# Optimization experiments

Hardware: AMD Instinct MI355X
Metric: run time of the kernel (lower is better)

Reference implementation:

```python
import jax, jax.numpy as jnp
import numpy as np

H, L, NB = 128, 2048, 64  # features, seq len, half state size (conj-symmetric N=128)


def _forward(u, x_re, x_im, Lambda_re, Lambda_im, B_re, B_im, C_re, C_im, D, d):
    Lam = (Lambda_re + 1j * Lambda_im).astype(jnp.complex64)   # (H, NB) discrete diag A
    B = (B_re + 1j * B_im).astype(jnp.complex64)               # (H, NB)
    C = (C_re + 1j * C_im).astype(jnp.complex64)               # (H, NB)
    x0 = (x_re + 1j * x_im).astype(jnp.complex64)              # (H, NB) initial state
    Hn, Ln = u.shape
    # scan elements (A_t, b_t, d_t); identity element (1, x0, False) prepended at t=0
    A = jnp.concatenate([jnp.ones((Hn, 1, NB), jnp.complex64),
                         jnp.broadcast_to(Lam[:, None, :], (Hn, Ln, NB))], axis=1)
    b = jnp.concatenate([x0[:, None, :],
                         B[:, None, :] * u[:, :, None].astype(jnp.complex64)], axis=1)
    dd = jnp.concatenate([jnp.zeros((1,), bool), d.astype(bool)])[None, :, None]  # (1, L+1, 1)

    def combine(lhs, rhs):
        # reset-aware associative combine: if right done-flag set, drop left contribution
        A_i, b_i, c_i = lhs
        A_j, b_j, c_j = rhs
        return (jnp.where(c_j, A_j, A_j * A_i),
                jnp.where(c_j, b_j, A_j * b_i + b_j),
                jnp.logical_or(c_i, c_j))

    _, xs, _ = jax.lax.associative_scan(combine, (A, b, dd), axis=1)
    xs = xs[:, 1:]                                             # (H, L, NB) hidden states
    # conj symmetry: y_t = 2*Re(C @ x_t) + D * u_t
    y = 2.0 * jnp.real(jnp.einsum('hn,hln->hl', C, xs)) + D[:, None] * u
    return y, xs[:, -1]


def setup_inputs():
    key = jax.random.key(0)
    ks = jax.random.split(key, 8)
    # stable ZOH-discretized HiPPO-like diagonal system (mirrors LSSL-f init)
    dts = jnp.logspace(-3.0, -1.0, H)                          # (H,) per-feature timescales
    k = jnp.arange(NB, dtype=jnp.float32)
    lam_c = -0.5 + 1j * jnp.pi * (2.0 * k + 1.0)               # (NB,) continuous poles
    lam_d = jnp.exp(dts[:, None] * lam_c[None, :]).astype(jnp.complex64)  # (H, NB), |.|<1
    Bc = ((jax.random.normal(ks[0], (NB,)) + 1j * jax.random.normal(ks[1], (NB,)))
          / jnp.sqrt(2.0 * NB)).astype(jnp.complex64)
    Bd = (((lam_d - 1.0) / lam_c[None, :]) * Bc[None, :]).astype(jnp.complex64)  # (H, NB)
    C = ((jax.random.normal(ks[2], (H, NB)) + 1j * jax.random.normal(ks[3], (H, NB)))
         / jnp.sqrt(float(NB))).astype(jnp.complex64)
    return {
        "u": jax.random.normal(ks[4], (H, L), jnp.float32),
        "x_re": jnp.zeros((H, NB), jnp.float32),
        "x_im": jnp.zeros((H, NB), jnp.float32),
        "Lambda_re": jnp.real(lam_d).astype(jnp.float32),
        "Lambda_im": jnp.imag(lam_d).astype(jnp.float32),
        "B_re": jnp.real(Bd).astype(jnp.float32),
        "B_im": jnp.imag(Bd).astype(jnp.float32),
        "C_re": jnp.real(C).astype(jnp.float32),
        "C_im": jnp.imag(C).astype(jnp.float32),
        "D": jax.random.normal(ks[5], (H,), jnp.float32),
        "d": jax.random.bernoulli(ks[6], 0.01, (L,)),
    }


def reference(u, x_re, x_im, Lambda_re, Lambda_im, B_re, B_im, C_re, C_im, D, d):
    return _forward(u, x_re, x_im, Lambda_re, Lambda_im, B_re, B_im, C_re, C_im, D, d)
```

## Files before the change

kernel.cpp:

```cpp
#include <hip/hip_runtime.h>

#define Hn 128
#define Ln 2048
#define NBn 64
#define K 64
#define G 32
#define PITCH 65


__global__ __launch_bounds__(64) void k1_summary(
    const float* __restrict__ u,
    const float* __restrict__ Lre,  const float* __restrict__ Lim,
    const float* __restrict__ Bre,  const float* __restrict__ Bim,
    const float* __restrict__ Cre,  const float* __restrict__ Cim,
    const int* __restrict__ dflag,
    float4* __restrict__ Sum)
{
    __shared__ float u_s[K];

    const int g = blockIdx.x, h = blockIdx.y, n = threadIdx.x;
    const int hn = h * NBn + n;
    const int l0 = g * K;

    const float lre = Lre[hn], lim = Lim[hn];
    const float br  = Bre[hn], bi  = Bim[hn];
    const float cr  = Cre[hn], ci  = Cim[hn];
    const float cbr2 = 2.f * (cr * br - ci * bi);
    const float cbi2 = 2.f * (cr * bi + ci * br);

    u_s[n] = u[h * Ln + l0 + n];
    const unsigned long long m = __ballot(dflag[l0 + n] != 0);
    __syncthreads();

    float wr = 0.f, wi = 0.f;
    if (m == 0ull) {
        #pragma unroll
        for (int k = 0; k < K; ++k) {
            const float uk = u_s[k];
            const float nr = fmaf(lre, wr, fmaf(-lim, wi, cbr2 * uk));
            const float ni = fmaf(lre, wi, fmaf( lim, wr, cbi2 * uk));
            wr = nr; wi = ni;
        }
    } else {
        #pragma unroll
        for (int k = 0; k < K; ++k) {
            const bool  rs  = (m >> k) & 1ull;
            const float lrk = rs ? 0.f : lre;
            const float lik = rs ? 0.f : lim;
            const float uk  = u_s[k];
            const float nr = fmaf(lrk, wr, fmaf(-lik, wi, cbr2 * uk));
            const float ni = fmaf(lrk, wi, fmaf( lik, wr, cbi2 * uk));
            wr = nr; wi = ni;
        }
    }

    float pr = lre, pi = lim;
    #pragma unroll
    for (int it = 0; it < 6; ++it) {
        const float sr2 = pr * pr - pi * pi;
        const float si2 = 2.f * pr * pi;
        pr = sr2; pi = si2;
    }
    if (m) { pr = 0.f; pi = 0.f; }
    Sum[(h * G + g) * NBn + n] = make_float4(pr, pi, wr, wi);
}

__global__ __launch_bounds__(64) void k2_combine(
    const float* __restrict__ x_re, const float* __restrict__ x_im,
    const float* __restrict__ Cre,  const float* __restrict__ Cim,
    const float4* __restrict__ Sum,
    float2* __restrict__ Sin,
    float* __restrict__ out)
{
    const int h = blockIdx.x, n = threadIdx.x;
    const int hn = h * NBn + n;
    const float cr = Cre[hn], ci = Cim[hn];
    const float x0r = x_re[hn], x0i = x_im[hn];
    float sre = 2.f * (cr * x0r - ci * x0i);
    float sim = 2.f * (cr * x0i + ci * x0r);
    #pragma unroll
    for (int g = 0; g < G; ++g) {
        const int idx = (h * G + g) * NBn + n;
        const float4 s = Sum[idx];
        Sin[idx] = make_float2(sre, sim);
        const float nr = fmaf(s.x, sre, fmaf(-s.y, sim, s.z));
        const float ni = fmaf(s.x, sim, fmaf( s.y, sre, s.w));
        sre = nr; sim = ni;
    }
    const float c2r = 2.f * cr, c2i = 2.f * ci;
    const float inv = 1.f / (c2r * c2r + c2i * c2i);
    float* xlast = out + Hn * Ln;
    xlast[2 * hn + 0] = (sre * c2r + sim * c2i) * inv;
    xlast[2 * hn + 1] = (sim * c2r - sre * c2i) * inv;
}

__global__ __launch_bounds__(64) void k3_rescan(
    const float* __restrict__ u,
    const float* __restrict__ Lre,  const float* __restrict__ Lim,
    const float* __restrict__ Bre,  const float* __restrict__ Bim,
    const float* __restrict__ Cre,  const float* __restrict__ Cim,
    const float* __restrict__ Dv,   const int* __restrict__ dflag,
    const float2* __restrict__ Sin,
    float* __restrict__ out)
{
    __shared__ float g_s[K * PITCH];
    __shared__ float u_s[K];

    const int g = blockIdx.x, h = blockIdx.y, n = threadIdx.x;
    const int hn = h * NBn + n;
    const int l0 = g * K;

    const float lre = Lre[hn], lim = Lim[hn];
    const float br  = Bre[hn], bi  = Bim[hn];
    const float cr  = Cre[hn], ci  = Cim[hn];
    const float Dh  = Dv[h];
    const float cbr2 = 2.f * (cr * br - ci * bi);
    const float cbi2 = 2.f * (cr * bi + ci * br);

    const float2 win = Sin[(h * G + g) * NBn + n];
    const float ul = u[h * Ln + l0 + n];
    u_s[n] = ul;
    const unsigned long long m = __ballot(dflag[l0 + n] != 0);
    __syncthreads();

    float wr = win.x, wi = win.y;
    if (m == 0ull) {
        #pragma unroll
        for (int k = 0; k < K; ++k) {
            const float uk = u_s[k];
            const float nr = fmaf(lre, wr, fmaf(-lim, wi, cbr2 * uk));
            const float ni = fmaf(lre, wi, fmaf( lim, wr, cbi2 * uk));
            wr = nr; wi = ni;
            g_s[k * PITCH + n] = wr;
        }
    } else {
        #pragma unroll
        for (int k = 0; k < K; ++k) {
            const bool  rs  = (m >> k) & 1ull;
            const float lrk = rs ? 0.f : lre;
            const float lik = rs ? 0.f : lim;
            const float uk  = u_s[k];
            const float nr = fmaf(lrk, wr, fmaf(-lik, wi, cbr2 * uk));
            const float ni = fmaf(lrk, wi, fmaf( lik, wr, cbi2 * uk));
            wr = nr; wi = ni;
            g_s[k * PITCH + n] = wr;
        }
    }
    __syncthreads();

    const float* row = g_s + n * PITCH;
    float a0 = 0.f, a1 = 0.f, a2 = 0.f, a3 = 0.f;
    #pragma unroll
    for (int k = 0; k < NBn; k += 4) {
        a0 += row[k + 0]; a1 += row[k + 1];
        a2 += row[k + 2]; a3 += row[k + 3];
    }
    out[h * Ln + l0 + n] = (a0 + a1) + (a2 + a3) + Dh * ul;
}

extern "C" void kernel_launch(void* const* d_in, const int* in_sizes, int n_in,
                              void* d_out, int out_size, void* d_ws, size_t ws_size,
                              hipStream_t stream) {
    const float* u    = (const float*)d_in[0];
    const float* x_re = (const float*)d_in[1];
    const float* x_im = (const float*)d_in[2];
    const float* Lre  = (const float*)d_in[3];
    const float* Lim  = (const float*)d_in[4];
    const float* Bre  = (const float*)d_in[5];
    const float* Bim  = (const float*)d_in[6];
    const float* Cre  = (const float*)d_in[7];
    const float* Cim  = (const float*)d_in[8];
    const float* Dv   = (const float*)d_in[9];
    const int*   dfl  = (const int*)d_in[10];
    float* out = (float*)d_out;

    const int HGN = Hn * G * NBn;
    float4* Sum = (float4*)d_ws;
    float2* Sin = (float2*)(Sum + HGN);

    dim3 grid(G, Hn);
    k1_summary<<<grid, 64, 0, stream>>>(u, Lre, Lim, Bre, Bim, Cre, Cim,
                                        dfl, Sum);
    k2_combine<<<Hn, 64, 0, stream>>>(x_re, x_im, Cre, Cim, Sum, Sin, out);
    k3_rescan<<<grid, 64, 0, stream>>>(u, Lre, Lim, Bre, Bim, Cre, Cim,
                                       Dv, dfl, Sin, out);
}
```

Measured before the change: 89.07 us.

## Fuse chunk summary and cross-chunk combine into one per-feature block

Merges the chunk-summary kernel and the sequential combine kernel into a single 1024-thread block per feature. Each of 16 waves computes two chunk summaries into shared memory, and wave 0 then runs the 32-step carry propagation from LDS. This removes one kernel launch and the global round-trip of the float4 summary buffer. In exchange, the first stage now runs only 128 blocks instead of 4096, and the serial combine runs on a single wave while the other 15 waves sit idle.

```diff
diff --git a/kernel.cpp b/kernel.cpp
--- a/kernel.cpp
+++ b/kernel.cpp
@@ -8,19 +8,22 @@
 #define PITCH 65
 
 
-__global__ __launch_bounds__(64) void k1_summary(
+__global__ __launch_bounds__(1024) void kA_sum_combine(
     const float* __restrict__ u,
+    const float* __restrict__ x_re, const float* __restrict__ x_im,
     const float* __restrict__ Lre,  const float* __restrict__ Lim,
     const float* __restrict__ Bre,  const float* __restrict__ Bim,
     const float* __restrict__ Cre,  const float* __restrict__ Cim,
     const int* __restrict__ dflag,
-    float4* __restrict__ Sum)
+    float2* __restrict__ Sin,
+    float* __restrict__ out)
 {
-    __shared__ float u_s[K];
+    __shared__ float  u_s[Ln];
+    __shared__ float4 b_s[G][NBn];
 
-    const int g = blockIdx.x, h = blockIdx.y, n = threadIdx.x;
+    const int h = blockIdx.x, tid = threadIdx.x;
+    const int w = tid >> 6, n = tid & 63;
     const int hn = h * NBn + n;
-    const int l0 = g * K;
 
     const float lre = Lre[hn], lim = Lim[hn];
     const float br  = Bre[hn], bi  = Bim[hn];
@@ -28,73 +31,78 @@
     const float cbr2 = 2.f * (cr * br - ci * bi);
     const float cbi2 = 2.f * (cr * bi + ci * br);
 
-    u_s[n] = u[h * Ln + l0 + n];
-    const unsigned long long m = __ballot(dflag[l0 + n] != 0);
+    u_s[tid]        = u[h * Ln + tid];
+    u_s[tid + 1024] = u[h * Ln + tid + 1024];
+
+    unsigned long long mk[2];
+    #pragma unroll
+    for (int jj = 0; jj < 2; ++jj)
+        mk[jj] = __ballot(dflag[(2 * w + jj) * K + n] != 0);
+
+    float l64r = lre, l64i = lim;
+    #pragma unroll
+    for (int it = 0; it < 6; ++it) {
+        const float a  = l64r * l64r - l64i * l64i;
+        const float b2 = 2.f * l64r * l64i;
+        l64r = a; l64i = b2;
+    }
+
     __syncthreads();
 
-    float wr = 0.f, wi = 0.f;
-    if (m == 0ull) {
+    #pragma unroll
+    for (int jj = 0; jj < 2; ++jj) {
+        const int j  = 2 * w + jj;
+        const int l0 = j * K;
+        const unsigned long long m = mk[jj];
+        float wr = 0.f, wi = 0.f;
+        if (m == 0ull) {
+            #pragma unroll
+            for (int k = 0; k < K; ++k) {
+                const float uk = u_s[l0 + k];
+                const float nr = fmaf(lre, wr, fmaf(-lim, wi, cbr2 * uk));
+                const float ni = fmaf(lre, wi, fmaf( lim, wr, cbi2 * uk));
+                wr = nr; wi = ni;
+            }
+        } else {
+            #pragma unroll
+            for (int k = 0; k < K; ++k) {
+                const bool  rs  = (m >> k) & 1ull;
+                const float lrk = rs ? 0.f : lre;
+                const float lik = rs ? 0.f : lim;
+                const float uk  = u_s[l0 + k];
+                const float nr = fmaf(lrk, wr, fmaf(-lik, wi, cbr2 * uk));
+                const float ni = fmaf(lrk, wi, fmaf( lik, wr, cbi2 * uk));
+                wr = nr; wi = ni;
+            }
+        }
+        const float ar = m ? 0.f : l64r;
+        const float ai = m ? 0.f : l64i;
+        b_s[j][n] = make_float4(ar, ai, wr, wi);
+    }
+    __syncthreads();
+
+    if (w == 0) {
+        const float x0r = x_re[hn], x0i = x_im[hn];
+        float sre = 2.f * (cr * x0r - ci * x0i);
+        float sim = 2.f * (cr * x0i + ci * x0r);
+        float2* sbase = Sin + h * G * NBn + n;
         #pragma unroll
-        for (int k = 0; k < K; ++k) {
-            const float uk = u_s[k];
-            const float nr = fmaf(lre, wr, fmaf(-lim, wi, cbr2 * uk));
-            const float ni = fmaf(lre, wi, fmaf( lim, wr, cbi2 * uk));
-            wr = nr; wi = ni;
+        for (int g = 0; g < G; ++g) {
+            const float4 s = b_s[g][n];
+            sbase[g * NBn] = make_float2(sre, sim);
+            const float nr = fmaf(s.x, sre, fmaf(-s.y, sim, s.z));
+            const float ni = fmaf(s.x, sim, fmaf( s.y, sre, s.w));
+            sre = nr; sim = ni;
         }
-    } else {
-        #pragma unroll
-        for (int k = 0; k < K; ++k) {
-            const bool  rs  = (m >> k) & 1ull;
-            const float lrk = rs ? 0.f : lre;
-            const float lik = rs ? 0.f : lim;
-            const float uk  = u_s[k];
-            const float nr = fmaf(lrk, wr, fmaf(-lik, wi, cbr2 * uk));
-            const float ni = fmaf(lrk, wi, fmaf( lik, wr, cbi2 * uk));
-            wr = nr; wi = ni;
-        }
+        const float c2r = 2.f * cr, c2i = 2.f * ci;
+        const float inv = 1.f / (c2r * c2r + c2i * c2i);
+        float* xlast = out + Hn * Ln;
+        xlast[2 * hn + 0] = (sre * c2r + sim * c2i) * inv;
+        xlast[2 * hn + 1] = (sim * c2r - sre * c2i) * inv;
     }
-
-    float pr = lre, pi = lim;
-    #pragma unroll
-    for (int it = 0; it < 6; ++it) {
-        const float sr2 = pr * pr - pi * pi;
-        const float si2 = 2.f * pr * pi;
-        pr = sr2; pi = si2;
-    }
-    if (m) { pr = 0.f; pi = 0.f; }
-    Sum[(h * G + g) * NBn + n] = make_float4(pr, pi, wr, wi);
 }
 
-__global__ __launch_bounds__(64) void k2_combine(
-    const float* __restrict__ x_re, const float* __restrict__ x_im,
-    const float* __restrict__ Cre,  const float* __restrict__ Cim,
-    const float4* __restrict__ Sum,
-    float2* __restrict__ Sin,
-    float* __restrict__ out)
-{
-    const int h = blockIdx.x, n = threadIdx.x;
-    const int hn = h * NBn + n;
-    const float cr = Cre[hn], ci = Cim[hn];
-    const float x0r = x_re[hn], x0i = x_im[hn];
-    float sre = 2.f * (cr * x0r - ci * x0i);
-    float sim = 2.f * (cr * x0i + ci * x0r);
-    #pragma unroll
-    for (int g = 0; g < G; ++g) {
-        const int idx = (h * G + g) * NBn + n;
-        const float4 s = Sum[idx];
-        Sin[idx] = make_float2(sre, sim);
-        const float nr = fmaf(s.x, sre, fmaf(-s.y, sim, s.z));
-        const float ni = fmaf(s.x, sim, fmaf( s.y, sre, s.w));
-        sre = nr; sim = ni;
-    }
-    const float c2r = 2.f * cr, c2i = 2.f * ci;
-    const float inv = 1.f / (c2r * c2r + c2i * c2i);
-    float* xlast = out + Hn * Ln;
-    xlast[2 * hn + 0] = (sre * c2r + sim * c2i) * inv;
-    xlast[2 * hn + 1] = (sim * c2r - sre * c2i) * inv;
-}
-
-__global__ __launch_bounds__(64) void k3_rescan(
+__global__ __launch_bounds__(64) void kB_rescan(
     const float* __restrict__ u,
     const float* __restrict__ Lre,  const float* __restrict__ Lim,
     const float* __restrict__ Bre,  const float* __restrict__ Bim,
@@ -174,14 +182,12 @@
     const int*   dfl  = (const int*)d_in[10];
     float* out = (float*)d_out;
 
-    const int HGN = Hn * G * NBn;
-    float4* Sum = (float4*)d_ws;
-    float2* Sin = (float2*)(Sum + HGN);
+    float2* Sin = (float2*)d_ws;
 
-    dim3 grid(G, Hn);
-    k1_summary<<<grid, 64, 0, stream>>>(u, Lre, Lim, Bre, Bim, Cre, Cim,
-                                        dfl, Sum);
-    k2_combine<<<Hn, 64, 0, stream>>>(x_re, x_im, Cre, Cim, Sum, Sin, out);
-    k3_rescan<<<grid, 64, 0, stream>>>(u, Lre, Lim, Bre, Bim, Cre, Cim,
-                                       Dv, dfl, Sin, out);
+    kA_sum_combine<<<Hn, 1024, 0, stream>>>(u, x_re, x_im, Lre, Lim,
+                                            Bre, Bim, Cre, Cim, dfl,
+                                            Sin, out);
+    dim3 gridB(G, Hn);
+    kB_rescan<<<gridB, 64, 0, stream>>>(u, Lre, Lim, Bre, Bim, Cre, Cim,
+                                        Dv, dfl, Sin, out);
 }
```

After: 89.02 us. No clear change (-0.1%).
